# Performance work log

Hardware: AMD Instinct MI355X
Metric: run time of the kernel (lower is better)

## Reference

```python
import jax, jax.numpy as jnp
import numpy as np

N_MBED = 384
HEAD_SIZE = 64

def setup_inputs() -> dict:
    key = jax.random.key(0)
    kx, kq, kk, kv = jax.random.split(key, 4)
    B, T = 128, 256
    x = jax.random.normal(kx, (B, T, N_MBED), dtype=jnp.float32)
    # torch nn.Linear(n_mbed, head_size, bias=False): y = x @ W^T, W:[head_size, n_mbed].
    # We store the transposed weight [n_mbed, head_size] so y = x @ W.
    s = 1.0 / np.sqrt(N_MBED)
    Wq = jax.random.uniform(kq, (N_MBED, HEAD_SIZE), jnp.float32, -s, s)
    Wk = jax.random.uniform(kk, (N_MBED, HEAD_SIZE), jnp.float32, -s, s)
    Wv = jax.random.uniform(kv, (N_MBED, HEAD_SIZE), jnp.float32, -s, s)
    return {"x": x, "Wq": Wq, "Wk": Wk, "Wv": Wv}

def reference(x, Wq, Wk, Wv):
    B, T, C = x.shape  # C = n_mbed = 384
    q = x @ Wq  # [B,T,H]
    k = x @ Wk
    v = x @ Wv
    # Faithful to source: wei = k @ q^T, scaled by C**-0.5 (C = n_mbed, not head_size)
    wei = jnp.einsum('bth,bsh->bts', k, q) * (C ** -0.5)  # [B,T,T]
    mask = jnp.tril(jnp.ones((T, T), dtype=bool))
    wei = jnp.where(mask, wei, -jnp.inf)
    wei = jax.nn.softmax(wei, axis=-1)
    # dropout omitted (eval mode / identity)
    out = jnp.einsum('bts,bsh->bth', wei, v)  # [B,T,H]
    return out
```

## Files before the change

kernel.cpp:

```cpp
#include <hip/hip_runtime.h>
#include <hip/hip_bf16.h>
#include <math.h>

constexpr int kB = 128;
constexpr int kT = 256;
constexpr int kC = 384;
constexpr int kH = 64;

using bf16x8 = __attribute__((ext_vector_type(8))) short;
using f32x4  = __attribute__((ext_vector_type(4))) float;

union BF4 { short4 s; __hip_bfloat162 h[2]; };

__device__ inline short4 cvt4(float4 a) {
    BF4 u;
    u.h[0] = __float22bfloat162_rn(float2{a.x, a.y});
    u.h[1] = __float22bfloat162_rn(float2{a.z, a.w});
    return u.s;
}
__device__ inline short bf1(float f) {
    __hip_bfloat16 h = __float2bfloat16(f);
    return *(short*)&h;
}

__global__ void prep_kernel(const float* __restrict__ Wq,
                            const float* __restrict__ Wk,
                            const float* __restrict__ Wv,
                            __hip_bfloat16* __restrict__ Wt) {
    int idx = blockIdx.x * 256 + threadIdx.x;
    int n = idx / kC, c = idx % kC;
    int w = n >> 6, h = n & 63;
    const float* W = (w == 0) ? Wq : (w == 1) ? Wk : Wv;
    float val = W[c * kH + h];
    if (w == 1) val *= 0.051031036307982884f;
    Wt[idx] = __float2bfloat16(val);
}

__global__ __launch_bounds__(512, 2) void fused_kernel(
    const float* __restrict__ x, const __hip_bfloat16* __restrict__ Wt,
    float* __restrict__ out)
{
    __shared__ short Qs[256 * 72];
    __shared__ short Ks[128 * 72];
    __shared__ short VTs[64 * 264];
    __shared__ short As[2][256 * 36];
    __shared__ short Bs[2][192 * 36];

    const int bid  = blockIdx.x;
    const int b    = ((bid >> 4) << 3) | (bid & 7);
    const int half = ((bid >> 3) & 1) ^ 1;
    const int t0   = half * 128;

    const int tid  = threadIdx.x;
    const int wave = tid >> 6, lane = tid & 63;
    const int m16  = lane & 15, quad = lane >> 4;
    const int wm = wave & 1, wn = wave >> 1;
    const short* wt = (const short*)Wt;
    const float* xb = x + (size_t)b * kT * kC;

    const bool mfmaAct = (half == 1) || (wm == 0);

    bool kskip[3];
#pragma unroll
    for (int j = 0; j < 3; ++j) {
        const int nt = wn * 3 + j;
        kskip[j] = (half == 1) && (wm == 0) && (nt >= 4) && (nt < 8);
    }

    const int arow = tid >> 1, acol = (tid & 1) * 16;
    const bool aAct = (half == 1) || (arow < 128);

    float4 la0[4], la1[4]; bf16x8 lb0a, lb0b, lb1a, lb1b;
    auto glod = [&](float4* la, bf16x8& lba, bf16x8& lbb, int k0) {
        if (aAct) {
#pragma unroll
            for (int i = 0; i < 4; ++i)
                la[i] = *(const float4*)(xb + (size_t)arow * kC + k0 + acol + 4 * i);
        }
        {
            int n = tid >> 2, kk = (tid & 3) * 8;
            lba = *(const bf16x8*)(wt + (size_t)n * kC + k0 + kk);
        }
        if (tid < 256) {
            int c = tid + 512;
            int n = c >> 2, kk = (c & 3) * 8;
            lbb = *(const bf16x8*)(wt + (size_t)n * kC + k0 + kk);
        }
    };
    auto swr = [&](int d, const float4* la, const bf16x8& lba, const bf16x8& lbb) {
        if (aAct) {
#pragma unroll
            for (int i = 0; i < 4; ++i)
                *(short4*)&As[d][arow * 36 + acol + 4 * i] = cvt4(la[i]);
        }
        {
            int n = tid >> 2, kk = (tid & 3) * 8;
            *(bf16x8*)&Bs[d][n * 36 + kk] = lba;
        }
        if (tid < 256) {
            int c = tid + 512;
            int n = c >> 2, kk = (c & 3) * 8;
            *(bf16x8*)&Bs[d][n * 36 + kk] = lbb;
        }
    };

    f32x4 acc[8][3];
#pragma unroll
    for (int mt = 0; mt < 8; ++mt)
#pragma unroll
        for (int j = 0; j < 3; ++j) acc[mt][j] = f32x4{0.f, 0.f, 0.f, 0.f};

    auto mstep = [&](int d) {
        if (!mfmaAct) return;
        bf16x8 af[8];
#pragma unroll
        for (int mt = 0; mt < 8; ++mt)
            af[mt] = *(const bf16x8*)&As[d][(wm * 128 + mt * 16 + m16) * 36 + quad * 8];
#pragma unroll
        for (int j = 0; j < 3; ++j) {
            if (!kskip[j]) {
                const bf16x8 bfr =
                    *(const bf16x8*)&Bs[d][((wn * 3 + j) * 16 + m16) * 36 + quad * 8];
#pragma unroll
                for (int mt = 0; mt < 8; ++mt)
                    acc[mt][j] = __builtin_amdgcn_mfma_f32_16x16x32_bf16(
                        af[mt], bfr, acc[mt][j], 0, 0, 0);
            }
        }
    };

    glod(la0, lb0a, lb0b, 0);
    glod(la1, lb1a, lb1b, 32);
    swr(0, la0, lb0a, lb0b);
    __syncthreads();

    for (int s = 0; s < 12; s += 2) {
        if (s < 10) glod(la0, lb0a, lb0b, (s + 2) * 32);
        mstep(0);
        swr(1, la1, lb1a, lb1b);
        __syncthreads();
        if (s + 1 < 10) glod(la1, lb1a, lb1b, (s + 3) * 32);
        mstep(1);
        if (s + 1 < 11) swr(0, la0, lb0a, lb0b);
        __syncthreads();
    }

    if (mfmaAct) {
#pragma unroll
        for (int mt = 0; mt < 8; ++mt) {
            const int mbase = wm * 128 + mt * 16 + quad * 4;
#pragma unroll
            for (int j = 0; j < 3; ++j) {
                const int nt = wn * 3 + j;
                const int w  = nt >> 2;
                const int h  = (nt & 3) * 16 + m16;
                if (w == 2) {
                    float4 f = make_float4(acc[mt][j][0], acc[mt][j][1],
                                           acc[mt][j][2], acc[mt][j][3]);
                    *(short4*)&VTs[h * 264 + mbase] = cvt4(f);
                } else if (w == 1) {
                    if ((mbase >> 7) == half) {
#pragma unroll
                        for (int r = 0; r < 4; ++r)
                            Ks[(mbase + r - t0) * 72 + h] = bf1(acc[mt][j][r]);
                    }
                } else {
#pragma unroll
                    for (int r = 0; r < 4; ++r)
                        Qs[(mbase + r) * 72 + h] = bf1(acc[mt][j][r]);
                }
            }
        }
    }
    __syncthreads();

    const int wband = t0 + wave * 16;
    short* Pb = &As[0][0] + wave * 1152;

    const bf16x8 ka0 = *(const bf16x8*)&Ks[(wave * 16 + m16) * 72 + quad * 8];
    const bf16x8 ka1 = *(const bf16x8*)&Ks[(wave * 16 + m16) * 72 + quad * 8 + 32];

    f32x4 O[4];
#pragma unroll
    for (int i = 0; i < 4; ++i) O[i] = f32x4{0.f, 0.f, 0.f, 0.f};
    float m_ = -INFINITY, l_ = 0.f;

    const int ilast = wband >> 6;
    for (int i = 0; i <= ilast; ++i) {
        const bool diag = (i == ilast);
        const int jmax = diag ? (wave & 3) : 3;

        f32x4 S[4];
        const f32x4 Z = f32x4{0.f, 0.f, 0.f, 0.f};
        __builtin_amdgcn_s_setprio(1);
#pragma unroll
        for (int j = 0; j < 4; ++j) {
            if (j <= jmax) {
                const int s = i * 64 + j * 16 + m16;
                bf16x8 qb0 = *(const bf16x8*)&Qs[s * 72 + quad * 8];
                bf16x8 qb1 = *(const bf16x8*)&Qs[s * 72 + quad * 8 + 32];
                S[j] = __builtin_amdgcn_mfma_f32_16x16x32_bf16(qb0, ka0, Z, 0, 0, 0);
                S[j] = __builtin_amdgcn_mfma_f32_16x16x32_bf16(qb1, ka1, S[j], 0, 0, 0);
            }
        }
        __builtin_amdgcn_s_setprio(0);
        if (diag) {
#pragma unroll
            for (int r = 0; r < 4; ++r)
                if (quad * 4 + r > m16) S[jmax][r] = -INFINITY;
        }

        float rm = -INFINITY;
#pragma unroll
        for (int j = 0; j < 4; ++j)
            if (j <= jmax)
#pragma unroll
                for (int r = 0; r < 4; ++r) rm = fmaxf(rm, S[j][r]);
        rm = fmaxf(rm, __shfl_xor(rm, 16, 64));
        rm = fmaxf(rm, __shfl_xor(rm, 32, 64));

        const float mn = fmaxf(m_, rm);
        const float al = __expf(m_ - mn);
        m_ = mn;

        float P[4][4];
#pragma unroll
        for (int j = 0; j < 4; ++j)
#pragma unroll
            for (int r = 0; r < 4; ++r) P[j][r] = 0.f;
        float rs = 0.f;
#pragma unroll
        for (int j = 0; j < 4; ++j) {
            if (j <= jmax) {
#pragma unroll
                for (int r = 0; r < 4; ++r) {
                    P[j][r] = __expf(S[j][r] - mn);
                    rs += P[j][r];
                }
            }
        }
        rs += __shfl_xor(rs, 16, 64);
        rs += __shfl_xor(rs, 32, 64);
        l_ = l_ * al + rs;

        float albc[4];
#pragma unroll
        for (int r = 0; r < 4; ++r)
            albc[r] = __shfl(al, (quad << 4) | (quad * 4 + r), 64);
#pragma unroll
        for (int ht = 0; ht < 4; ++ht)
#pragma unroll
            for (int r = 0; r < 4; ++r) O[ht][r] *= albc[r];

#pragma unroll
        for (int j = 0; j < 4; ++j)
#pragma unroll
            for (int p = 0; p < 2; ++p) {
                __hip_bfloat162 w =
                    __float22bfloat162_rn(float2{P[j][2 * p], P[j][2 * p + 1]});
                *(__hip_bfloat162*)&Pb[m16 * 72 + j * 16 + quad * 4 + 2 * p] = w;
            }
        bf16x8 pf0 = *(const bf16x8*)&Pb[m16 * 72 + quad * 8];
        bf16x8 pf1 = *(const bf16x8*)&Pb[m16 * 72 + quad * 8 + 32];

        __builtin_amdgcn_s_setprio(1);
#pragma unroll
        for (int ht = 0; ht < 4; ++ht) {
            bf16x8 vb0 = *(const bf16x8*)&VTs[(ht * 16 + m16) * 264 + i * 64 + quad * 8];
            bf16x8 vb1 = *(const bf16x8*)&VTs[(ht * 16 + m16) * 264 + i * 64 + quad * 8 + 32];
            O[ht] = __builtin_amdgcn_mfma_f32_16x16x32_bf16(pf0, vb0, O[ht], 0, 0, 0);
            O[ht] = __builtin_amdgcn_mfma_f32_16x16x32_bf16(pf1, vb1, O[ht], 0, 0, 0);
        }
        __builtin_amdgcn_s_setprio(0);
    }

    float lbc[4];
#pragma unroll
    for (int r = 0; r < 4; ++r)
        lbc[r] = __shfl(l_, (quad << 4) | (quad * 4 + r), 64);
#pragma unroll
    for (int r = 0; r < 4; ++r) {
        const float inv = 1.f / lbc[r];
        const size_t row = (size_t)(b * kT + wband + quad * 4 + r);
#pragma unroll
        for (int ht = 0; ht < 4; ++ht)
            out[row * kH + ht * 16 + m16] = O[ht][r] * inv;
    }
}

extern "C" void kernel_launch(void* const* d_in, const int* in_sizes, int n_in,
                              void* d_out, int out_size, void* d_ws, size_t ws_size,
                              hipStream_t stream) {
    const float* x  = (const float*)d_in[0];
    const float* Wq = (const float*)d_in[1];
    const float* Wk = (const float*)d_in[2];
    const float* Wv = (const float*)d_in[3];
    float* out = (float*)d_out;

    __hip_bfloat16* Wt = (__hip_bfloat16*)d_ws;

    prep_kernel<<<(192 * kC) / 256, 256, 0, stream>>>(Wq, Wk, Wv, Wt);
    fused_kernel<<<dim3(256), 512, 0, stream>>>(x, Wt, out);
}
```

Before: 114.4 us.

## Replace online softmax with full-row two-pass softmax held in registers

Since T is only 256, all score tiles for a wave's 16-row band fit in registers, so the kernel now computes every score tile first. It then takes a single row max, exponentiates and sums once, and finally runs the PV MFMAs. This removes the per-block rescaling of the output accumulator, the repeated max/sum shuffles and the alpha broadcasts. The cost is a 64-float score array per lane, which raises register pressure and may reduce occupancy or cause spills. Loops are fully unrolled with runtime guards.

```diff
diff --git a/kernel.cpp b/kernel.cpp
--- a/kernel.cpp
+++ b/kernel.cpp
@@ -180,98 +180,98 @@
     const bf16x8 ka0 = *(const bf16x8*)&Ks[(wave * 16 + m16) * 72 + quad * 8];
     const bf16x8 ka1 = *(const bf16x8*)&Ks[(wave * 16 + m16) * 72 + quad * 8 + 32];
 
+    const int ilast = wband >> 6;
+    const int jmaxd = wave & 3;
+
+    f32x4 S[4][4];
+    const f32x4 Z = f32x4{0.f, 0.f, 0.f, 0.f};
+#pragma unroll
+    for (int i = 0; i < 4; ++i)
+#pragma unroll
+        for (int j = 0; j < 4; ++j) S[i][j] = Z;
+
+    __builtin_amdgcn_s_setprio(1);
+#pragma unroll
+    for (int i = 0; i < 4; ++i) {
+        if (i <= ilast) {
+#pragma unroll
+            for (int j = 0; j < 4; ++j) {
+                if (i < ilast || j <= jmaxd) {
+                    const int s = i * 64 + j * 16 + m16;
+                    bf16x8 qb0 = *(const bf16x8*)&Qs[s * 72 + quad * 8];
+                    bf16x8 qb1 = *(const bf16x8*)&Qs[s * 72 + quad * 8 + 32];
+                    S[i][j] = __builtin_amdgcn_mfma_f32_16x16x32_bf16(qb0, ka0, S[i][j], 0, 0, 0);
+                    S[i][j] = __builtin_amdgcn_mfma_f32_16x16x32_bf16(qb1, ka1, S[i][j], 0, 0, 0);
+                }
+            }
+        }
+    }
+    __builtin_amdgcn_s_setprio(0);
+
+#pragma unroll
+    for (int i = 0; i < 4; ++i)
+#pragma unroll
+        for (int j = 0; j < 4; ++j)
+            if (i == ilast && j == jmaxd) {
+#pragma unroll
+                for (int r = 0; r < 4; ++r)
+                    if (quad * 4 + r > m16) S[i][j][r] = -INFINITY;
+            }
+
+    float rm = -INFINITY;
+#pragma unroll
+    for (int i = 0; i < 4; ++i)
+#pragma unroll
+        for (int j = 0; j < 4; ++j)
+            if (i <= ilast && (i < ilast || j <= jmaxd))
+#pragma unroll
+                for (int r = 0; r < 4; ++r) rm = fmaxf(rm, S[i][j][r]);
+    rm = fmaxf(rm, __shfl_xor(rm, 16, 64));
+    rm = fmaxf(rm, __shfl_xor(rm, 32, 64));
+
+    float l_ = 0.f;
+#pragma unroll
+    for (int i = 0; i < 4; ++i)
+#pragma unroll
+        for (int j = 0; j < 4; ++j)
+            if (i <= ilast && (i < ilast || j <= jmaxd))
+#pragma unroll
+                for (int r = 0; r < 4; ++r) {
+                    const float e = __expf(S[i][j][r] - rm);
+                    S[i][j][r] = e;
+                    l_ += e;
+                }
+    l_ += __shfl_xor(l_, 16, 64);
+    l_ += __shfl_xor(l_, 32, 64);
+
     f32x4 O[4];
 #pragma unroll
     for (int i = 0; i < 4; ++i) O[i] = f32x4{0.f, 0.f, 0.f, 0.f};
-    float m_ = -INFINITY, l_ = 0.f;
-
-    const int ilast = wband >> 6;
-    for (int i = 0; i <= ilast; ++i) {
-        const bool diag = (i == ilast);
-        const int jmax = diag ? (wave & 3) : 3;
-
-        f32x4 S[4];
-        const f32x4 Z = f32x4{0.f, 0.f, 0.f, 0.f};
-        __builtin_amdgcn_s_setprio(1);
-#pragma unroll
-        for (int j = 0; j < 4; ++j) {
-            if (j <= jmax) {
-                const int s = i * 64 + j * 16 + m16;
-                bf16x8 qb0 = *(const bf16x8*)&Qs[s * 72 + quad * 8];
-                bf16x8 qb1 = *(const bf16x8*)&Qs[s * 72 + quad * 8 + 32];
-                S[j] = __builtin_amdgcn_mfma_f32_16x16x32_bf16(qb0, ka0, Z, 0, 0, 0);
-                S[j] = __builtin_amdgcn_mfma_f32_16x16x32_bf16(qb1, ka1, S[j], 0, 0, 0);
-            }
-        }
-        __builtin_amdgcn_s_setprio(0);
-        if (diag) {
-#pragma unroll
-            for (int r = 0; r < 4; ++r)
-                if (quad * 4 + r > m16) S[jmax][r] = -INFINITY;
-        }
-
-        float rm = -INFINITY;
-#pragma unroll
-        for (int j = 0; j < 4; ++j)
-            if (j <= jmax)
-#pragma unroll
-                for (int r = 0; r < 4; ++r) rm = fmaxf(rm, S[j][r]);
-        rm = fmaxf(rm, __shfl_xor(rm, 16, 64));
-        rm = fmaxf(rm, __shfl_xor(rm, 32, 64));
-
-        const float mn = fmaxf(m_, rm);
-        const float al = __expf(m_ - mn);
-        m_ = mn;
-
-        float P[4][4];
-#pragma unroll
-        for (int j = 0; j < 4; ++j)
-#pragma unroll
-            for (int r = 0; r < 4; ++r) P[j][r] = 0.f;
-        float rs = 0.f;
-#pragma unroll
-        for (int j = 0; j < 4; ++j) {
-            if (j <= jmax) {
-#pragma unroll
-                for (int r = 0; r < 4; ++r) {
-                    P[j][r] = __expf(S[j][r] - mn);
-                    rs += P[j][r];
+
+#pragma unroll
+    for (int i = 0; i < 4; ++i) {
+        if (i <= ilast) {
+#pragma unroll
+            for (int j = 0; j < 4; ++j)
+#pragma unroll
+                for (int p = 0; p < 2; ++p) {
+                    __hip_bfloat162 w = __float22bfloat162_rn(
+                        float2{S[i][j][2 * p], S[i][j][2 * p + 1]});
+                    *(__hip_bfloat162*)&Pb[m16 * 72 + j * 16 + quad * 4 + 2 * p] = w;
                 }
-            }
-        }
-        rs += __shfl_xor(rs, 16, 64);
-        rs += __shfl_xor(rs, 32, 64);
-        l_ = l_ * al + rs;
-
-        float albc[4];
-#pragma unroll
-        for (int r = 0; r < 4; ++r)
-            albc[r] = __shfl(al, (quad << 4) | (quad * 4 + r), 64);
-#pragma unroll
-        for (int ht = 0; ht < 4; ++ht)
-#pragma unroll
-            for (int r = 0; r < 4; ++r) O[ht][r] *= albc[r];
-
-#pragma unroll
-        for (int j = 0; j < 4; ++j)
-#pragma unroll
-            for (int p = 0; p < 2; ++p) {
-                __hip_bfloat162 w =
-                    __float22bfloat162_rn(float2{P[j][2 * p], P[j][2 * p + 1]});
-                *(__hip_bfloat162*)&Pb[m16 * 72 + j * 16 + quad * 4 + 2 * p] = w;
-            }
-        bf16x8 pf0 = *(const bf16x8*)&Pb[m16 * 72 + quad * 8];
-        bf16x8 pf1 = *(const bf16x8*)&Pb[m16 * 72 + quad * 8 + 32];
-
-        __builtin_amdgcn_s_setprio(1);
-#pragma unroll
-        for (int ht = 0; ht < 4; ++ht) {
-            bf16x8 vb0 = *(const bf16x8*)&VTs[(ht * 16 + m16) * 264 + i * 64 + quad * 8];
-            bf16x8 vb1 = *(const bf16x8*)&VTs[(ht * 16 + m16) * 264 + i * 64 + quad * 8 + 32];
-            O[ht] = __builtin_amdgcn_mfma_f32_16x16x32_bf16(pf0, vb0, O[ht], 0, 0, 0);
-            O[ht] = __builtin_amdgcn_mfma_f32_16x16x32_bf16(pf1, vb1, O[ht], 0, 0, 0);
-        }
-        __builtin_amdgcn_s_setprio(0);
+            bf16x8 pf0 = *(const bf16x8*)&Pb[m16 * 72 + quad * 8];
+            bf16x8 pf1 = *(const bf16x8*)&Pb[m16 * 72 + quad * 8 + 32];
+
+            __builtin_amdgcn_s_setprio(1);
+#pragma unroll
+            for (int ht = 0; ht < 4; ++ht) {
+                bf16x8 vb0 = *(const bf16x8*)&VTs[(ht * 16 + m16) * 264 + i * 64 + quad * 8];
+                bf16x8 vb1 = *(const bf16x8*)&VTs[(ht * 16 + m16) * 264 + i * 64 + quad * 8 + 32];
+                O[ht] = __builtin_amdgcn_mfma_f32_16x16x32_bf16(pf0, vb0, O[ht], 0, 0, 0);
+                O[ht] = __builtin_amdgcn_mfma_f32_16x16x32_bf16(pf1, vb1, O[ht], 0, 0, 0);
+            }
+            __builtin_amdgcn_s_setprio(0);
+        }
     }
 
     float lbc[4];
```

Measured after the change: 110.7 us. 1.03x faster.
